# Kernel optimization log

Measured on AMD Instinct MI355X. Metric: run time of the kernel, lower is better.

Reference implementation:

```python
import jax, jax.numpy as jnp
import numpy as np

N = 100000   # nodes
E = 1600000  # edges
D = 128      # input_dim == hidden_dim
L = 3        # num_layers
G = 256      # graphs in batch
EPS = 1e-5   # BatchNorm eps


def setup_inputs() -> dict:
    key = jax.random.key(0)
    ks = jax.random.split(key, 10)
    x = jax.random.normal(ks[0], (N, D), dtype=jnp.float32)
    edge_index = jax.random.randint(ks[1], (2, E), 0, N, dtype=jnp.int64)
    batch = jnp.sort(jax.random.randint(ks[2], (N,), 0, G, dtype=jnp.int64))
    # stacked per-layer params (all layers are D->D since input_dim==hidden_dim)
    W = jax.random.normal(ks[3], (L, D, D), dtype=jnp.float32) * 0.05
    b = jax.random.normal(ks[4], (L, D), dtype=jnp.float32) * 0.02
    gamma = 1.0 + 0.1 * jax.random.normal(ks[5], (L, D), dtype=jnp.float32)
    beta = 0.1 * jax.random.normal(ks[6], (L, D), dtype=jnp.float32)
    rmean = 0.05 * jax.random.normal(ks[7], (L, D), dtype=jnp.float32)
    rvar = jax.random.uniform(ks[8], (L, D), minval=0.5, maxval=1.5, dtype=jnp.float32)
    return {"x": x, "W": W, "b": b, "gamma": gamma, "beta": beta,
            "rmean": rmean, "rvar": rvar, "edge_index": edge_index, "batch": batch}


def reference(x, W, b, gamma, beta, rmean, rvar, edge_index, batch):
    # --- GCN normalization with self-loops (same for every layer) ---
    src, dst = edge_index[0], edge_index[1]
    loop = jnp.arange(N, dtype=src.dtype)
    s = jnp.concatenate([src, loop])  # [E+N]
    d = jnp.concatenate([dst, loop])
    deg = jax.ops.segment_sum(jnp.ones(E + N, x.dtype), d, num_segments=N)
    dinv = jnp.where(deg > 0, jax.lax.rsqrt(deg), 0.0)
    norm = dinv[s] * dinv[d]  # [E+N]

    h = x
    for i in range(L):
        m = h @ W[i]                                            # [N, D] dense GEMM
        agg = jax.ops.segment_sum(m[s] * norm[:, None], d, num_segments=N)
        h = agg + b[i]
        # BatchNorm1d (inference: running stats), then ReLU; dropout is identity in eval
        h = (h - rmean[i]) * jax.lax.rsqrt(rvar[i] + EPS) * gamma[i] + beta[i]
        h = jax.nn.relu(h)

    # --- global mean / max pooling by graph id ---
    counts = jax.ops.segment_sum(jnp.ones(N, h.dtype), batch, num_segments=G)
    mean_pool = jax.ops.segment_sum(h, batch, num_segments=G) / jnp.maximum(counts, 1.0)[:, None]
    max_pool = jax.ops.segment_max(h, batch, num_segments=G)
    return jnp.concatenate([mean_pool, max_pool], axis=1)  # [G, 2D]
```

## Files before the change

### kernel.cpp

```cpp
#include <hip/hip_runtime.h>
#include <math.h>
#include <float.h>

#define D 128

typedef short short8 __attribute__((ext_vector_type(8)));
typedef float f32x4 __attribute__((ext_vector_type(4)));

__device__ __forceinline__ unsigned int bf16r(float f) {
    unsigned int u = __float_as_uint(f);
    return (u + 0x7fffu + ((u >> 16) & 1u)) >> 16;
}
__device__ __forceinline__ float bf2f(unsigned int lo16) {
    return __uint_as_float(lo16 << 16);
}

__global__ __launch_bounds__(256) void prep_fused(
    const int* __restrict__ dst, int* __restrict__ cnt, int* __restrict__ rank, int E,
    const float* __restrict__ W, const float* __restrict__ b,
    const float* __restrict__ gamma, const float* __restrict__ beta,
    const float* __restrict__ rmean, const float* __restrict__ rvar,
    unsigned short* __restrict__ Wt, float* __restrict__ sc, float* __restrict__ sh, int L_,
    const int* __restrict__ batch, int* __restrict__ gstart, int n, int G,
    int cb, int wb) {
    int blk = blockIdx.x;
    int tid = threadIdx.x;
    if (blk < cb) {
        int base = (blk * 256 + tid) * 4;
        if (base + 4 <= E) {
            int4 d = *(const int4*)&dst[base];
            int r0 = atomicAdd(&cnt[d.x], 1);
            int r1 = atomicAdd(&cnt[d.y], 1);
            int r2 = atomicAdd(&cnt[d.z], 1);
            int r3 = atomicAdd(&cnt[d.w], 1);
            *(int4*)&rank[base] = make_int4(r0, r1, r2, r3);
        } else if (base < E) {
            for (int e = base; e < E; ++e) rank[e] = atomicAdd(&cnt[dst[e]], 1);
        }
    } else if (blk < cb + wb) {
        int t = (blk - cb) * 256 + tid;
        int total = L_ * D * D;
        if (t < total) {
            int l = t / (D * D), rem = t % (D * D);
            int r = rem >> 7, k = rem & 127;
            Wt[t] = (unsigned short)bf16r(W[l * D * D + k * D + r]);
        }
        if (t < L_ * D) {
            float inv = rsqrtf(rvar[t] + 1e-5f);
            float s = inv * gamma[t];
            sc[t] = s;
            sh[t] = (b[t] - rmean[t]) * s + beta[t];
        }
    } else {
        int i = (blk - cb - wb) * 256 + tid;
        if (i >= n) return;
        int g = batch[i];
        int gp = (i == 0) ? -1 : batch[i - 1];
        for (int gg = gp + 1; gg <= g; ++gg) gstart[gg] = i;
        if (i == n - 1) for (int gg = g + 1; gg <= G; ++gg) gstart[gg] = n;
    }
}


__global__ void scan1(const int* __restrict__ cnt, int* __restrict__ rp, int* __restrict__ aux,
                      float* __restrict__ dinv, int n) {
    __shared__ int sh[256];
    int tid = threadIdx.x;
    int base = blockIdx.x * 1024 + tid * 4;
    int v[4]; int s = 0;
#pragma unroll
    for (int i = 0; i < 4; i++) {
        int idx = base + i;
        int t = (idx < n) ? cnt[idx] : 0;
        if (idx < n) dinv[idx] = rsqrtf((float)t + 1.0f);
        v[i] = s; s += t;
    }
    sh[tid] = s; __syncthreads();
    for (int off = 1; off < 256; off <<= 1) {
        int t = (tid >= off) ? sh[tid - off] : 0;
        __syncthreads();
        sh[tid] += t;
        __syncthreads();
    }
    int excl = sh[tid] - s;
#pragma unroll
    for (int i = 0; i < 4; i++) { int idx = base + i; if (idx < n) rp[idx] = excl + v[i]; }
    if (tid == 255) aux[blockIdx.x] = sh[255];
}

__global__ void scan2(int* aux, int nb) {
    __shared__ int sh[256];
    int tid = threadIdx.x;
    int v = (tid < nb) ? aux[tid] : 0;
    sh[tid] = v; __syncthreads();
    for (int off = 1; off < 256; off <<= 1) {
        int t = (tid >= off) ? sh[tid - off] : 0;
        __syncthreads();
        sh[tid] += t;
        __syncthreads();
    }
    if (tid < nb) aux[tid] = sh[tid] - v;
}

#define GBM 128
__device__ __forceinline__ void gemm0_body(short* Wl, const float* __restrict__ x,
                                           const unsigned short* __restrict__ Wt,
                                           const float* __restrict__ dinv,
                                           unsigned short* __restrict__ mout, int n, int blk) {
    const int tid = threadIdx.x;
    const int row0 = blk * GBM;

#pragma unroll
    for (int i = 0; i < 4; ++i) {
        int c = tid + i * 512;
        int r = c >> 4, ck = (c & 15) * 8;
        *(int4*)&Wl[r * 136 + ck] = *(const int4*)&Wt[(size_t)r * D + ck];
    }
    __syncthreads();

    const int wid = tid >> 6;
    const int lane = tid & 63;
    const int lr = lane & 15;
    const int lg = lane >> 4;

    const int grow = row0 + wid * 16 + lr;
    const bool valid = grow < n;

    f32x4 acc[8];
#pragma unroll
    for (int fc = 0; fc < 8; ++fc) acc[fc] = (f32x4){0.f, 0.f, 0.f, 0.f};

#pragma unroll
    for (int ks = 0; ks < 4; ++ks) {
        int kb = ks * 32 + lg * 8;
        float4 va = make_float4(0.f, 0.f, 0.f, 0.f);
        float4 vb = make_float4(0.f, 0.f, 0.f, 0.f);
        if (valid) {
            va = *(const float4*)&x[(size_t)grow * D + kb];
            vb = *(const float4*)&x[(size_t)grow * D + kb + 4];
        }
        uint4 pk;
        pk.x = bf16r(va.x) | (bf16r(va.y) << 16);
        pk.y = bf16r(va.z) | (bf16r(va.w) << 16);
        pk.z = bf16r(vb.x) | (bf16r(vb.y) << 16);
        pk.w = bf16r(vb.z) | (bf16r(vb.w) << 16);
        short8 y = *(short8*)&pk;
#pragma unroll
        for (int fc = 0; fc < 8; ++fc) {
            short8 xf = *(const short8*)&Wl[(fc * 16 + lr) * 136 + kb];
            acc[fc] = __builtin_amdgcn_mfma_f32_16x16x32_bf16(xf, y, acc[fc], 0, 0, 0);
        }
    }

    if (valid) {
        float di = dinv[grow];
#pragma unroll
        for (int fc = 0; fc < 8; ++fc) {
            int gcol = fc * 16 + lg * 4;
            uint2 pk;
            pk.x = bf16r(acc[fc][0] * di) | (bf16r(acc[fc][1] * di) << 16);
            pk.y = bf16r(acc[fc][2] * di) | (bf16r(acc[fc][3] * di) << 16);
            *(uint2*)&mout[(size_t)grow * D + gcol] = pk;
        }
    }
}

__global__ __launch_bounds__(512) void fused_fill_gemm0(
    const float* __restrict__ x, const unsigned short* __restrict__ Wt,
    const float* __restrict__ dinv, unsigned short* __restrict__ mout, int n,
    const int* __restrict__ src, const int* __restrict__ dst,
    const int* __restrict__ rp, const int* __restrict__ aux,
    const int* __restrict__ rank, int* __restrict__ csr, int E, int gemmb) {
    __shared__ short Wl[D * 136];
    if ((int)blockIdx.x < gemmb) {
        gemm0_body(Wl, x, Wt, dinv, mout, n, blockIdx.x);
    } else {
        int gblk = blockIdx.x - gemmb;
        int base = (gblk * 512 + (int)threadIdx.x) * 4;
        if (base + 4 <= E) {
            int4 d = *(const int4*)&dst[base];
            int4 s = *(const int4*)&src[base];
            int4 r = *(const int4*)&rank[base];
            int p0 = rp[d.x] + aux[d.x >> 10];
            int p1 = rp[d.y] + aux[d.y >> 10];
            int p2 = rp[d.z] + aux[d.z >> 10];
            int p3 = rp[d.w] + aux[d.w >> 10];
            csr[p0 + r.x] = s.x;
            csr[p1 + r.y] = s.y;
            csr[p2 + r.z] = s.z;
            csr[p3 + r.w] = s.w;
        } else if (base < E) {
            for (int e = base; e < E; ++e)
                csr[rp[dst[e]] + aux[dst[e] >> 10] + rank[e]] = src[e];
        }
    }
}

__global__ __launch_bounds__(512) void gemm_mfma(const unsigned short* __restrict__ hin,
                                                 const unsigned short* __restrict__ Wt,
                                                 const float* __restrict__ dinv,
                                                 unsigned short* __restrict__ mout, int n) {
    __shared__ short Wl[D * 136];
    const int tid = threadIdx.x;
    const int row0 = blockIdx.x * GBM;

#pragma unroll
    for (int i = 0; i < 4; ++i) {
        int c = tid + i * 512;
        int r = c >> 4, ck = (c & 15) * 8;
        *(int4*)&Wl[r * 136 + ck] = *(const int4*)&Wt[(size_t)r * D + ck];
    }
    __syncthreads();

    const int wid = tid >> 6;
    const int lane = tid & 63;
    const int lr = lane & 15;
    const int lg = lane >> 4;

    const int grow = row0 + wid * 16 + lr;
    const bool valid = grow < n;

    f32x4 acc[8];
#pragma unroll
    for (int fc = 0; fc < 8; ++fc) acc[fc] = (f32x4){0.f, 0.f, 0.f, 0.f};

#pragma unroll
    for (int ks = 0; ks < 4; ++ks) {
        int kb = ks * 32 + lg * 8;
        short8 y;
        if (valid) y = *(const short8*)&hin[(size_t)grow * D + kb];
        else { int4 z = make_int4(0, 0, 0, 0); y = *(short8*)&z; }
#pragma unroll
        for (int fc = 0; fc < 8; ++fc) {
            short8 xf = *(const short8*)&Wl[(fc * 16 + lr) * 136 + kb];
            acc[fc] = __builtin_amdgcn_mfma_f32_16x16x32_bf16(xf, y, acc[fc], 0, 0, 0);
        }
    }

    if (valid) {
        float di = dinv[grow];
#pragma unroll
        for (int fc = 0; fc < 8; ++fc) {
            int gcol = fc * 16 + lg * 4;
            uint2 pk;
            pk.x = bf16r(acc[fc][0] * di) | (bf16r(acc[fc][1] * di) << 16);
            pk.y = bf16r(acc[fc][2] * di) | (bf16r(acc[fc][3] * di) << 16);
            *(uint2*)&mout[(size_t)grow * D + gcol] = pk;
        }
    }
}

__global__ __launch_bounds__(256) void agg_bf16(const unsigned int* __restrict__ M,
                                                const int* __restrict__ rp,
                                                const int* __restrict__ aux,
                                                const int* __restrict__ csr,
                                                const float* __restrict__ dinv,
                                                const float* __restrict__ sc,
                                                const float* __restrict__ sh,
                                                unsigned int* __restrict__ H, int n, int Etot) {
    const int wid = threadIdx.x >> 6;
    const int lane = threadIdx.x & 63;
    const int row = blockIdx.x * 4 + wid;
    if (row >= n) return;

    unsigned int u = M[(unsigned)row * 64u + lane];
    float a0 = bf2f(u & 0xffffu);
    float a1 = bf2f(u >> 16);

    int e = rp[row] + aux[row >> 10];
    const int end = (row + 1 < n) ? rp[row + 1] + aux[(row + 1) >> 10] : Etot;
    const int n16 = (end - e) >> 4;

    if (n16 > 0) {
        int sa[16];
#pragma unroll
        for (int i = 0; i < 16; ++i) sa[i] = csr[e + i];
        for (int it = 0; it < n16; ++it) {
            int sb[16];
            if (it + 1 < n16) {
#pragma unroll
                for (int i = 0; i < 16; ++i) sb[i] = csr[e + 16 + i];
            } else {
#pragma unroll
                for (int i = 0; i < 16; ++i) sb[i] = 0;
            }
            unsigned int g[16];
#pragma unroll
            for (int i = 0; i < 16; ++i) g[i] = M[(unsigned)sa[i] * 64u + lane];
#pragma unroll
            for (int i = 0; i < 16; ++i) {
                a0 += bf2f(g[i] & 0xffffu);
                a1 += bf2f(g[i] >> 16);
            }
#pragma unroll
            for (int i = 0; i < 16; ++i) sa[i] = sb[i];
            e += 16;
        }
    }
    for (; e + 4 <= end; e += 4) {
        int s[4];
#pragma unroll
        for (int i = 0; i < 4; ++i) s[i] = csr[e + i];
        unsigned int g[4];
#pragma unroll
        for (int i = 0; i < 4; ++i) g[i] = M[(unsigned)s[i] * 64u + lane];
#pragma unroll
        for (int i = 0; i < 4; ++i) {
            a0 += bf2f(g[i] & 0xffffu);
            a1 += bf2f(g[i] >> 16);
        }
    }
    for (; e < end; ++e) {
        unsigned int gs = M[(unsigned)csr[e] * 64u + lane];
        a0 += bf2f(gs & 0xffffu);
        a1 += bf2f(gs >> 16);
    }

    float di = dinv[row];
    int c0 = lane * 2;
    float v0 = fmaxf(a0 * di * sc[c0] + sh[c0], 0.f);
    float v1 = fmaxf(a1 * di * sc[c0 + 1] + sh[c0 + 1], 0.f);
    H[(unsigned)row * 64u + lane] = bf16r(v0) | (bf16r(v1) << 16);
}

__global__ __launch_bounds__(64) void pool1(const unsigned int* __restrict__ H,
                                            const int* __restrict__ gstart,
                                            float4* __restrict__ pbuf) {
    int g = blockIdx.x, c = blockIdx.y;
    int lane = threadIdx.x;
    int beg = gstart[g], end = gstart[g + 1];
    int len = end - beg;
    int cb = beg + (int)(((long long)len * c) >> 3);
    int ce = beg + (int)(((long long)len * (c + 1)) >> 3);
    float s0 = 0.f, s1 = 0.f, m0 = -INFINITY, m1 = -INFINITY;
    int i = cb;
    for (; i + 2 <= ce; i += 2) {
        unsigned int ua = H[(size_t)i * 64 + lane];
        unsigned int ub = H[(size_t)(i + 1) * 64 + lane];
        float a0 = bf2f(ua & 0xffffu), a1 = bf2f(ua >> 16);
        float b0 = bf2f(ub & 0xffffu), b1 = bf2f(ub >> 16);
        s0 += a0 + b0; s1 += a1 + b1;
        m0 = fmaxf(m0, fmaxf(a0, b0)); m1 = fmaxf(m1, fmaxf(a1, b1));
    }
    for (; i < ce; ++i) {
        unsigned int ua = H[(size_t)i * 64 + lane];
        float a0 = bf2f(ua & 0xffffu), a1 = bf2f(ua >> 16);
        s0 += a0; s1 += a1;
        m0 = fmaxf(m0, a0); m1 = fmaxf(m1, a1);
    }
    pbuf[((size_t)g * 8 + c) * 64 + lane] = make_float4(s0, s1, m0, m1);
}

__global__ __launch_bounds__(64) void pool2(const float4* __restrict__ pbuf,
                                            const int* __restrict__ gstart,
                                            float* __restrict__ out) {
    int g = blockIdx.x;
    int lane = threadIdx.x;
    float s0 = 0.f, s1 = 0.f, m0 = -INFINITY, m1 = -INFINITY;
#pragma unroll
    for (int c = 0; c < 8; ++c) {
        float4 p = pbuf[((size_t)g * 8 + c) * 64 + lane];
        s0 += p.x; s1 += p.y;
        m0 = fmaxf(m0, p.z); m1 = fmaxf(m1, p.w);
    }
    float cnt = fmaxf((float)(gstart[g + 1] - gstart[g]), 1.0f);
    int c0 = lane * 2;
    out[g * (2 * D) + c0] = s0 / cnt;
    out[g * (2 * D) + c0 + 1] = s1 / cnt;
    out[g * (2 * D) + D + c0] = m0;
    out[g * (2 * D) + D + c0 + 1] = m1;
}

extern "C" void kernel_launch(void* const* d_in, const int* in_sizes, int n_in,
                              void* d_out, int out_size, void* d_ws, size_t ws_size,
                              hipStream_t stream) {
    const float* x     = (const float*)d_in[0];
    const float* W     = (const float*)d_in[1];
    const float* b     = (const float*)d_in[2];
    const float* gamma = (const float*)d_in[3];
    const float* beta  = (const float*)d_in[4];
    const float* rmean = (const float*)d_in[5];
    const float* rvar  = (const float*)d_in[6];
    const int*   eidx  = (const int*)d_in[7];
    const int*   batch = (const int*)d_in[8];

    const int N = in_sizes[8];
    const int E = in_sizes[7] / 2;
    const int L = in_sizes[2] / D;
    const int G = out_size / (2 * D);

    const int* esrc = eidx;
    const int* edst = eidx + E;

    size_t off = 0;
    auto carve = [&](size_t bytes) { size_t cur = off; off += (bytes + 255) & ~(size_t)255; return cur; };
    char* base = (char*)d_ws;
    const int nb = (N + 1023) / 1024;

    int*            cnt  = (int*)           (base + carve((size_t)N * 4));
    int*            rp   = (int*)           (base + carve((size_t)(N + 1) * 4));
    int*            aux  = (int*)           (base + carve((size_t)nb * 4));
    float*          dinv = (float*)         (base + carve((size_t)N * 4));
    int*            rank = (int*)           (base + carve((size_t)E * 4));
    int*            csr  = (int*)           (base + carve((size_t)E * 4));
    unsigned short* hbuf = (unsigned short*)(base + carve((size_t)N * D * 2));
    unsigned short* mbuf = (unsigned short*)(base + carve((size_t)N * D * 2));
    unsigned short* Wt   = (unsigned short*)(base + carve((size_t)L * D * D * 2));
    float*          sc   = (float*)         (base + carve((size_t)L * D * 4));
    float*          shb  = (float*)         (base + carve((size_t)L * D * 4));
    int*            gst  = (int*)           (base + carve((size_t)(G + 1) * 4));
    float4*         pbuf = (float4*)        (base + carve((size_t)G * 8 * 64 * 16));
    (void)ws_size;

    hipMemsetAsync(cnt, 0, (size_t)N * 4, stream);

    const int cb = ((E + 3) / 4 + 255) / 256;
    const int wb = (L * D * D + 255) / 256;
    const int bb = (N + 255) / 256;
    const int gemmb = (N + GBM - 1) / GBM;
    const int fb = ((E + 3) / 4 + 511) / 512;
    const int aggb = (N + 3) / 4;

    prep_fused<<<cb + wb + bb, 256, 0, stream>>>(edst, cnt, rank, E,
                                                 W, b, gamma, beta, rmean, rvar,
                                                 Wt, sc, shb, L,
                                                 batch, gst, N, G, cb, wb);
    scan1<<<nb, 256, 0, stream>>>(cnt, rp, aux, dinv, N);
    scan2<<<1, 256, 0, stream>>>(aux, nb);

    fused_fill_gemm0<<<gemmb + fb, 512, 0, stream>>>(x, Wt, dinv, mbuf, N,
                                                     esrc, edst, rp, aux, rank, csr, E, gemmb);
    agg_bf16<<<aggb, 256, 0, stream>>>((const unsigned int*)mbuf, rp, aux, csr, dinv,
                                       sc, shb, (unsigned int*)hbuf, N, E);

    for (int l = 1; l < L; ++l) {
        gemm_mfma<<<gemmb, 512, 0, stream>>>(hbuf, Wt + (size_t)l * D * D, dinv, mbuf, N);
        agg_bf16<<<aggb, 256, 0, stream>>>((const unsigned int*)mbuf, rp, aux, csr, dinv,
                                           sc + l * D, shb + l * D,
                                           (unsigned int*)hbuf, N, E);
    }

    pool1<<<dim3(G, 8), 64, 0, stream>>>((const unsigned int*)hbuf, gst, pbuf);
    pool2<<<G, 64, 0, stream>>>(pbuf, gst, (float*)d_out);
}
```

Before: 362.1 us.

## Fuse layer aggregation with next layer's GEMM in a persistent tiled kernel

Aggregation of layer l (gather, BN, ReLU) and the GEMM of layer l+1 now run in one persistent kernel. Each block aggregates a 16-row tile into shared memory, then applies the next layer's weights with MFMA and writes the pre-scaled messages. This removes the intermediate hidden-state write and read plus two kernel launches. In exchange it adds per-tile block barriers, a 1024-block grid cap, and a heavier kernel whose random gathers may hide latency less well than the standalone aggregation kernel.

```diff
diff --git a/kernel.cpp b/kernel.cpp
--- a/kernel.cpp
+++ b/kernel.cpp
@@ -196,13 +196,76 @@
     }
 }
 
-__global__ __launch_bounds__(512) void gemm_mfma(const unsigned short* __restrict__ hin,
-                                                 const unsigned short* __restrict__ Wt,
-                                                 const float* __restrict__ dinv,
-                                                 unsigned short* __restrict__ mout, int n) {
+__device__ __forceinline__ void agg_row(const unsigned int* __restrict__ M,
+                                        const int* __restrict__ rp,
+                                        const int* __restrict__ aux,
+                                        const int* __restrict__ csr,
+                                        int row, int n, int Etot, int lane,
+                                        float& a0, float& a1) {
+    unsigned int u = M[(unsigned)row * 64u + lane];
+    a0 = bf2f(u & 0xffffu);
+    a1 = bf2f(u >> 16);
+
+    int e = rp[row] + aux[row >> 10];
+    const int end = (row + 1 < n) ? rp[row + 1] + aux[(row + 1) >> 10] : Etot;
+    const int n16 = (end - e) >> 4;
+
+    if (n16 > 0) {
+        int sa[16];
+#pragma unroll
+        for (int i = 0; i < 16; ++i) sa[i] = csr[e + i];
+        for (int it = 0; it < n16; ++it) {
+            int sb[16];
+            if (it + 1 < n16) {
+#pragma unroll
+                for (int i = 0; i < 16; ++i) sb[i] = csr[e + 16 + i];
+            } else {
+#pragma unroll
+                for (int i = 0; i < 16; ++i) sb[i] = 0;
+            }
+            unsigned int g[16];
+#pragma unroll
+            for (int i = 0; i < 16; ++i) g[i] = M[(unsigned)sa[i] * 64u + lane];
+#pragma unroll
+            for (int i = 0; i < 16; ++i) {
+                a0 += bf2f(g[i] & 0xffffu);
+                a1 += bf2f(g[i] >> 16);
+            }
+#pragma unroll
+            for (int i = 0; i < 16; ++i) sa[i] = sb[i];
+            e += 16;
+        }
+    }
+    for (; e + 4 <= end; e += 4) {
+        int s[4];
+#pragma unroll
+        for (int i = 0; i < 4; ++i) s[i] = csr[e + i];
+        unsigned int g[4];
+#pragma unroll
+        for (int i = 0; i < 4; ++i) g[i] = M[(unsigned)s[i] * 64u + lane];
+#pragma unroll
+        for (int i = 0; i < 4; ++i) {
+            a0 += bf2f(g[i] & 0xffffu);
+            a1 += bf2f(g[i] >> 16);
+        }
+    }
+    for (; e < end; ++e) {
+        unsigned int gs = M[(unsigned)csr[e] * 64u + lane];
+        a0 += bf2f(gs & 0xffffu);
+        a1 += bf2f(gs >> 16);
+    }
+}
+
+__global__ __launch_bounds__(512) void agg_gemm(
+    const unsigned int* __restrict__ M,
+    const int* __restrict__ rp, const int* __restrict__ aux,
+    const int* __restrict__ csr, const float* __restrict__ dinv,
+    const float* __restrict__ sc, const float* __restrict__ sh,
+    const unsigned short* __restrict__ Wt,
+    unsigned short* __restrict__ mout, int n, int Etot, int ntiles) {
     __shared__ short Wl[D * 136];
+    __shared__ short Hl[16 * 136];
     const int tid = threadIdx.x;
-    const int row0 = blockIdx.x * GBM;
 
 #pragma unroll
     for (int i = 0; i < 4; ++i) {
@@ -210,43 +273,53 @@
         int r = c >> 4, ck = (c & 15) * 8;
         *(int4*)&Wl[r * 136 + ck] = *(const int4*)&Wt[(size_t)r * D + ck];
     }
-    __syncthreads();
 
     const int wid = tid >> 6;
     const int lane = tid & 63;
     const int lr = lane & 15;
     const int lg = lane >> 4;
-
-    const int grow = row0 + wid * 16 + lr;
-    const bool valid = grow < n;
-
-    f32x4 acc[8];
-#pragma unroll
-    for (int fc = 0; fc < 8; ++fc) acc[fc] = (f32x4){0.f, 0.f, 0.f, 0.f};
-
-#pragma unroll
-    for (int ks = 0; ks < 4; ++ks) {
-        int kb = ks * 32 + lg * 8;
-        short8 y;
-        if (valid) y = *(const short8*)&hin[(size_t)grow * D + kb];
-        else { int4 z = make_int4(0, 0, 0, 0); y = *(short8*)&z; }
-#pragma unroll
-        for (int fc = 0; fc < 8; ++fc) {
-            short8 xf = *(const short8*)&Wl[(fc * 16 + lr) * 136 + kb];
-            acc[fc] = __builtin_amdgcn_mfma_f32_16x16x32_bf16(xf, y, acc[fc], 0, 0, 0);
-        }
-    }
-
-    if (valid) {
-        float di = dinv[grow];
-#pragma unroll
-        for (int fc = 0; fc < 8; ++fc) {
-            int gcol = fc * 16 + lg * 4;
+    const int c0 = lane * 2;
+    const float s0v = sc[c0], s1v = sc[c0 + 1];
+    const float h0v = sh[c0], h1v = sh[c0 + 1];
+
+    __syncthreads();
+
+    for (int tile = blockIdx.x; tile < ntiles; tile += gridDim.x) {
+        const int row0 = tile * 16;
+#pragma unroll
+        for (int rr = 0; rr < 2; ++rr) {
+            int rloc = wid * 2 + rr;
+            int row = row0 + rloc;
+            unsigned int hv = 0;
+            if (row < n) {
+                float a0, a1;
+                agg_row(M, rp, aux, csr, row, n, Etot, lane, a0, a1);
+                float di = dinv[row];
+                float v0 = fmaxf(a0 * di * s0v + h0v, 0.f);
+                float v1 = fmaxf(a1 * di * s1v + h1v, 0.f);
+                hv = bf16r(v0) | (bf16r(v1) << 16);
+            }
+            *(unsigned int*)&Hl[rloc * 136 + lane * 2] = hv;
+        }
+        __syncthreads();
+
+        f32x4 acc = (f32x4){0.f, 0.f, 0.f, 0.f};
+#pragma unroll
+        for (int ks = 0; ks < 4; ++ks) {
+            int kb = ks * 32 + lg * 8;
+            short8 y = *(const short8*)&Hl[lr * 136 + kb];
+            short8 xf = *(const short8*)&Wl[(wid * 16 + lr) * 136 + kb];
+            acc = __builtin_amdgcn_mfma_f32_16x16x32_bf16(xf, y, acc, 0, 0, 0);
+        }
+        int node = row0 + lr;
+        if (node < n) {
+            float di = dinv[node];
             uint2 pk;
-            pk.x = bf16r(acc[fc][0] * di) | (bf16r(acc[fc][1] * di) << 16);
-            pk.y = bf16r(acc[fc][2] * di) | (bf16r(acc[fc][3] * di) << 16);
-            *(uint2*)&mout[(size_t)grow * D + gcol] = pk;
-        }
+            pk.x = bf16r(acc[0] * di) | (bf16r(acc[1] * di) << 16);
+            pk.y = bf16r(acc[2] * di) | (bf16r(acc[3] * di) << 16);
+            *(uint2*)&mout[(size_t)node * D + wid * 16 + lg * 4] = pk;
+        }
+        __syncthreads();
     }
 }
 
@@ -263,58 +336,8 @@
     const int row = blockIdx.x * 4 + wid;
     if (row >= n) return;
 
-    unsigned int u = M[(unsigned)row * 64u + lane];
-    float a0 = bf2f(u & 0xffffu);
-    float a1 = bf2f(u >> 16);
-
-    int e = rp[row] + aux[row >> 10];
-    const int end = (row + 1 < n) ? rp[row + 1] + aux[(row + 1) >> 10] : Etot;
-    const int n16 = (end - e) >> 4;
-
-    if (n16 > 0) {
-        int sa[16];
-#pragma unroll
-        for (int i = 0; i < 16; ++i) sa[i] = csr[e + i];
-        for (int it = 0; it < n16; ++it) {
-            int sb[16];
-            if (it + 1 < n16) {
-#pragma unroll
-                for (int i = 0; i < 16; ++i) sb[i] = csr[e + 16 + i];
-            } else {
-#pragma unroll
-                for (int i = 0; i < 16; ++i) sb[i] = 0;
-            }
-            unsigned int g[16];
-#pragma unroll
-            for (int i = 0; i < 16; ++i) g[i] = M[(unsigned)sa[i] * 64u + lane];
-#pragma unroll
-            for (int i = 0; i < 16; ++i) {
-                a0 += bf2f(g[i] & 0xffffu);
-                a1 += bf2f(g[i] >> 16);
-            }
-#pragma unroll
-            for (int i = 0; i < 16; ++i) sa[i] = sb[i];
-            e += 16;
-        }
-    }
-    for (; e + 4 <= end; e += 4) {
-        int s[4];
-#pragma unroll
-        for (int i = 0; i < 4; ++i) s[i] = csr[e + i];
-        unsigned int g[4];
-#pragma unroll
-        for (int i = 0; i < 4; ++i) g[i] = M[(unsigned)s[i] * 64u + lane];
-#pragma unroll
-        for (int i = 0; i < 4; ++i) {
-            a0 += bf2f(g[i] & 0xffffu);
-            a1 += bf2f(g[i] >> 16);
-        }
-    }
-    for (; e < end; ++e) {
-        unsigned int gs = M[(unsigned)csr[e] * 64u + lane];
-        a0 += bf2f(gs & 0xffffu);
-        a1 += bf2f(gs >> 16);
-    }
+    float a0, a1;
+    agg_row(M, rp, aux, csr, row, n, Etot, lane, a0, a1);
 
     float di = dinv[row];
     int c0 = lane * 2;
@@ -403,8 +426,8 @@
     float*          dinv = (float*)         (base + carve((size_t)N * 4));
     int*            rank = (int*)           (base + carve((size_t)E * 4));
     int*            csr  = (int*)           (base + carve((size_t)E * 4));
-    unsigned short* hbuf = (unsigned short*)(base + carve((size_t)N * D * 2));
-    unsigned short* mbuf = (unsigned short*)(base + carve((size_t)N * D * 2));
+    unsigned short* bufA = (unsigned short*)(base + carve((size_t)N * D * 2));
+    unsigned short* bufB = (unsigned short*)(base + carve((size_t)N * D * 2));
     unsigned short* Wt   = (unsigned short*)(base + carve((size_t)L * D * D * 2));
     float*          sc   = (float*)         (base + carve((size_t)L * D * 4));
     float*          shb  = (float*)         (base + carve((size_t)L * D * 4));
@@ -420,6 +443,8 @@
     const int gemmb = (N + GBM - 1) / GBM;
     const int fb = ((E + 3) / 4 + 511) / 512;
     const int aggb = (N + 3) / 4;
+    const int ntiles = (N + 15) / 16;
+    const int agblocks = ntiles < 1024 ? ntiles : 1024;
 
     prep_fused<<<cb + wb + bb, 256, 0, stream>>>(edst, cnt, rank, E,
                                                  W, b, gamma, beta, rmean, rvar,
@@ -428,18 +453,19 @@
     scan1<<<nb, 256, 0, stream>>>(cnt, rp, aux, dinv, N);
     scan2<<<1, 256, 0, stream>>>(aux, nb);
 
-    fused_fill_gemm0<<<gemmb + fb, 512, 0, stream>>>(x, Wt, dinv, mbuf, N,
+    fused_fill_gemm0<<<gemmb + fb, 512, 0, stream>>>(x, Wt, dinv, bufA, N,
                                                      esrc, edst, rp, aux, rank, csr, E, gemmb);
-    agg_bf16<<<aggb, 256, 0, stream>>>((const unsigned int*)mbuf, rp, aux, csr, dinv,
-                                       sc, shb, (unsigned int*)hbuf, N, E);
-
-    for (int l = 1; l < L; ++l) {
-        gemm_mfma<<<gemmb, 512, 0, stream>>>(hbuf, Wt + (size_t)l * D * D, dinv, mbuf, N);
-        agg_bf16<<<aggb, 256, 0, stream>>>((const unsigned int*)mbuf, rp, aux, csr, dinv,
-                                           sc + l * D, shb + l * D,
-                                           (unsigned int*)hbuf, N, E);
-    }
-
-    pool1<<<dim3(G, 8), 64, 0, stream>>>((const unsigned int*)hbuf, gst, pbuf);
+
+    agg_gemm<<<agblocks, 512, 0, stream>>>((const unsigned int*)bufA, rp, aux, csr, dinv,
+                                           sc, shb, Wt + (size_t)1 * D * D,
+                                           bufB, N, E, ntiles);
+    agg_gemm<<<agblocks, 512, 0, stream>>>((const unsigned int*)bufB, rp, aux, csr, dinv,
+                                           sc + D, shb + D, Wt + (size_t)2 * D * D,
+                                           bufA, N, E, ntiles);
+    agg_bf16<<<aggb, 256, 0, stream>>>((const unsigned int*)bufA, rp, aux, csr, dinv,
+                                       sc + 2 * D, shb + 2 * D,
+                                       (unsigned int*)bufB, N, E);
+
+    pool1<<<dim3(G, 8), 64, 0, stream>>>((const unsigned int*)bufB, gst, pbuf);
     pool2<<<G, 64, 0, stream>>>(pbuf, gst, (float*)d_out);
 }
```

New measurement: 346.2 us. 4.4% less time.
